# Performance work log

Hardware: AMD Instinct MI355X
Metric: run time of the kernel (lower is better)

The kernel has to match this reference:

```python
import jax, jax.numpy as jnp
import numpy as np

B, E, O, H = 4096, 1024, 16, 1024  # batch, embed_dim, num_ops, hidden_dim


def setup_inputs() -> dict:
    key = jax.random.key(0)
    k1, k2, k3, k4, k5, k6 = jax.random.split(key, 6)
    s1 = 1.0 / np.sqrt(E)
    s2 = 1.0 / np.sqrt(H)
    return {
        "x_aug": jax.random.normal(k1, (B, E), dtype=jnp.float32),
        "op_idx": jax.random.randint(k2, (B,), 0, O, dtype=jnp.int32),
        "W1": jax.random.normal(k3, (E, O, H), dtype=jnp.float32) * s1,  # DenseGeneral kernel: embed -> (ops, hidden)
        "b1": jnp.zeros((O, H), dtype=jnp.float32),
        "W2": jax.random.normal(k4, (H, O, H), dtype=jnp.float32) * s2,  # per-op second layer (diagonal of DenseGeneral)
        "b2": jnp.zeros((O, H), dtype=jnp.float32),
    }


def reference(x_aug, op_idx, W1, b1, W2, b2):
    # h1[b,o,h] = relu(sum_e x[b,e] W1[e,o,h] + b1[o,h])
    h1 = jax.nn.relu(jnp.einsum("be,eoh->boh", x_aug, W1) + b1)
    # h2[b,o,g] = relu(sum_h h1[b,o,h] W2[h,o,g] + b2[o,g])  (per-op MLP)
    h2 = jax.nn.relu(jnp.einsum("boh,hog->bog", h1, W2) + b2)
    # select the chosen operator's output per example
    idx = jnp.broadcast_to(op_idx[:, None, None], (x_aug.shape[0], 1, h2.shape[-1]))
    return jnp.take_along_axis(h2, idx, axis=1).squeeze(1)  # [B, H]
```

## Files before the change

### kernel.cpp

```cpp
#include <hip/hip_runtime.h>

#define Bn 4096
#define En 1024
#define On 16
#define Hn 1024
#define MT 80

using floatx4 = __attribute__((ext_vector_type(4))) float;
using float4v = __attribute__((ext_vector_type(4))) float;
using bf16x8  = __attribute__((ext_vector_type(8))) __bf16;
using short8v = __attribute__((ext_vector_type(8))) short;

__device__ inline unsigned short f2bf(float f) {
    unsigned u = __builtin_bit_cast(unsigned, f);
    u += 0x7fffu + ((u >> 16) & 1u);
    return (unsigned short)(u >> 16);
}

#define GLOAD16(gp, lp) __builtin_amdgcn_global_load_lds( \
    (const __attribute__((address_space(1))) unsigned int*)(gp), \
    (__attribute__((address_space(3))) unsigned int*)(lp), 16, 0, 0)

__global__ __launch_bounds__(256) void wtrans_kernel(const float* __restrict__ W,
                                                     unsigned short* __restrict__ Wt,
                                                     const int* __restrict__ op_idx,
                                                     int* __restrict__ sidx_pad,
                                                     int* __restrict__ offs) {
    if (blockIdx.z == On) {
        if (blockIdx.x != 0 || blockIdx.y != 0) return;
        __shared__ int cnt[On], cur[On], po[On + 1];
        int tid = threadIdx.x;
        if (tid < On) { cnt[tid] = 0; cur[tid] = 0; }
        __syncthreads();
        for (int i = tid; i < Bn; i += 256) atomicAdd(&cnt[op_idx[i]], 1);
        __syncthreads();
        if (tid == 0) {
            int ps = 0;
            for (int o = 0; o < On; ++o) { po[o] = ps; ps += (cnt[o] + 63) & ~63; }
            po[On] = ps;
        }
        __syncthreads();
        for (int p = tid; p < MT * 64; p += 256) sidx_pad[p] = -1;
        __syncthreads();
        for (int i = tid; i < Bn; i += 256) {
            int o = op_idx[i];
            sidx_pad[po[o] + atomicAdd(&cur[o], 1)] = i;
        }
        if (tid <= On) offs[tid] = po[tid];
        if (tid < On)  offs[20 + tid] = cnt[tid];
        return;
    }
    __shared__ float tile[64][65];
    int o = blockIdx.z, e0 = blockIdx.y * 64, h0 = blockIdx.x * 64;
    int t = threadIdx.x;
    int er = t >> 4, c4 = (t & 15) * 4;
#pragma unroll
    for (int r = 0; r < 4; ++r) {
        const float* p = W + ((size_t)(e0 + er + 16 * r) * On + o) * Hn + h0 + c4;
        *(float4v*)&tile[er + 16 * r][c4] = *(const float4v*)p;
    }
    __syncthreads();
    int row = t & 63, gl = t >> 6;
#pragma unroll
    for (int r = 0; r < 2; ++r) {
        int ggl = gl + 4 * r;
        short8v v;
#pragma unroll
        for (int j = 0; j < 8; ++j) v[j] = (short)f2bf(tile[ggl * 8 + j][row]);
        int gg = (e0 >> 3) + ggl;
        size_t dst = ((((size_t)o * 8 + (h0 >> 7)) * 128 + gg) * 128 + ((h0 & 64) + row)) * 8;
        *(short8v*)(Wt + dst) = v;
    }
}

__global__ __launch_bounds__(256) void xprep_kernel(const float* __restrict__ x,
                                                    const int* __restrict__ sidx_pad,
                                                    const int* __restrict__ offs,
                                                    unsigned short* __restrict__ xs) {
    int p0 = blockIdx.x * 64;
    if (p0 >= offs[On]) return;
    int t = threadIdx.x, row = t & 63, gl = t >> 6;
    int src = sidx_pad[p0 + row];
    const float* xr = (src >= 0) ? (x + (size_t)src * En) : nullptr;
    unsigned short* xbase = xs + (size_t)(p0 >> 6) * 65536 + row * 8;
#pragma unroll 4
    for (int r = 0; r < 32; ++r) {
        int gg = gl + r * 4;
        short8v v = {};
        if (xr) {
            float4v f0 = *(const float4v*)(xr + gg * 8);
            float4v f1 = *(const float4v*)(xr + gg * 8 + 4);
#pragma unroll
            for (int j = 0; j < 4; ++j) { v[j] = (short)f2bf(f0[j]); v[4 + j] = (short)f2bf(f1[j]); }
        }
        *(short8v*)(xbase + (size_t)gg * 512) = v;
    }
}

__global__ __launch_bounds__(256, 4) void gemm1_kernel(
    const unsigned short* __restrict__ xs, const unsigned short* __restrict__ Wt,
    const float* __restrict__ bias1, const int* __restrict__ offs,
    unsigned short* __restrict__ h1T) {
    int o = blockIdx.z;
    int cnt = offs[20 + o];
    int m0 = blockIdx.y * 64;
    if (m0 >= cnt) return;
    int mtile = (offs[o] >> 6) + blockIdx.y;
    int n0 = blockIdx.x * 128;

    __shared__ unsigned short As[2][8][64][8];
    __shared__ unsigned short Bs[2][8][128][8];

    int tid = threadIdx.x, lane = tid & 63, wave = tid >> 6;
    const unsigned short* Abase = xs + (size_t)mtile * 65536 + lane * 8;
    const unsigned short* Bbase = Wt + ((size_t)o * 8 + (n0 >> 7)) * 131072 + lane * 8;

    floatx4 acc[2][4] = {};
    int wm = (wave >> 1) * 32, wn = (wave & 1) * 64;
    int l15 = lane & 15, kg = lane >> 4;

#pragma unroll
    for (int i = 0; i < 2; ++i) { int g = wave * 2 + i; GLOAD16(Abase + g * 512, &As[0][g][0][0]); }
#pragma unroll
    for (int i = 0; i < 4; ++i) { int idx = wave * 4 + i; int g = idx >> 1, hf = idx & 1;
        GLOAD16(Bbase + g * 1024 + hf * 512, &Bs[0][g][hf * 64][0]); }

    for (int it = 0; it < 16; ++it) {
        int cur = it & 1;
        __syncthreads();
        if (it + 1 < 16) {
            int aoff = (it + 1) * 4096, boff = (it + 1) * 8192;
#pragma unroll
            for (int i = 0; i < 2; ++i) { int g = wave * 2 + i;
                GLOAD16(Abase + aoff + g * 512, &As[cur ^ 1][g][0][0]); }
#pragma unroll
            for (int i = 0; i < 4; ++i) { int idx = wave * 4 + i; int g = idx >> 1, hf = idx & 1;
                GLOAD16(Bbase + boff + g * 1024 + hf * 512, &Bs[cur ^ 1][g][hf * 64][0]); }
        }
#pragma unroll
        for (int ks = 0; ks < 2; ++ks) {
            int g = ks * 4 + kg;
            bf16x8 af[2], bfr[4];
#pragma unroll
            for (int mt = 0; mt < 2; ++mt) af[mt] = *(const bf16x8*)&As[cur][g][wm + mt * 16 + l15][0];
#pragma unroll
            for (int nt = 0; nt < 4; ++nt) bfr[nt] = *(const bf16x8*)&Bs[cur][g][wn + nt * 16 + l15][0];
#pragma unroll
            for (int mt = 0; mt < 2; ++mt)
#pragma unroll
                for (int nt = 0; nt < 4; ++nt)
                    acc[mt][nt] = __builtin_amdgcn_mfma_f32_16x16x32_bf16(af[mt], bfr[nt], acc[mt][nt], 0, 0, 0);
        }
    }
    __syncthreads();

    unsigned short* ep = &As[0][0][0][0];
#pragma unroll
    for (int nt = 0; nt < 4; ++nt) {
        int col = wn + nt * 16 + l15;
        float bv = bias1[o * Hn + n0 + col];
#pragma unroll
        for (int mt = 0; mt < 2; ++mt)
#pragma unroll
            for (int r = 0; r < 4; ++r) {
                int rowl = wm + mt * 16 + kg * 4 + r;
                float v = acc[mt][nt][r] + bv;
                ep[((col >> 3) * 64 + rowl) * 8 + (col & 7)] = f2bf(v > 0.f ? v : 0.f);
            }
    }
    __syncthreads();
    unsigned short* dst = h1T + (size_t)mtile * 65536 + (size_t)(n0 >> 3) * 512;
#pragma unroll
    for (int rr = 0; rr < 4; ++rr) {
        int idx = rr * 256 + tid;
        *(short8v*)(dst + idx * 8) = *(const short8v*)(ep + idx * 8);
    }
}

__global__ __launch_bounds__(256, 4) void gemm2_kernel(
    const unsigned short* __restrict__ h1T, const unsigned short* __restrict__ Wt,
    const float* __restrict__ bias2, const int* __restrict__ sidx_pad,
    const int* __restrict__ offs, float* __restrict__ out) {
    int o = blockIdx.z;
    int cnt = offs[20 + o];
    int m0 = blockIdx.y * 64;
    if (m0 >= cnt) return;
    int mtile = (offs[o] >> 6) + blockIdx.y;
    int n0 = blockIdx.x * 128;

    __shared__ unsigned short As[2][8][64][8];
    __shared__ unsigned short Bs[2][8][128][8];

    int tid = threadIdx.x, lane = tid & 63, wave = tid >> 6;
    const unsigned short* Abase = h1T + (size_t)mtile * 65536 + lane * 8;
    const unsigned short* Bbase = Wt + ((size_t)o * 8 + (n0 >> 7)) * 131072 + lane * 8;

    floatx4 acc[2][4] = {};
    int wm = (wave >> 1) * 32, wn = (wave & 1) * 64;
    int l15 = lane & 15, kg = lane >> 4;

#pragma unroll
    for (int i = 0; i < 2; ++i) { int g = wave * 2 + i; GLOAD16(Abase + g * 512, &As[0][g][0][0]); }
#pragma unroll
    for (int i = 0; i < 4; ++i) { int idx = wave * 4 + i; int g = idx >> 1, hf = idx & 1;
        GLOAD16(Bbase + g * 1024 + hf * 512, &Bs[0][g][hf * 64][0]); }

    for (int it = 0; it < 16; ++it) {
        int cur = it & 1;
        __syncthreads();
        if (it + 1 < 16) {
            int aoff = (it + 1) * 4096, boff = (it + 1) * 8192;
#pragma unroll
            for (int i = 0; i < 2; ++i) { int g = wave * 2 + i;
                GLOAD16(Abase + aoff + g * 512, &As[cur ^ 1][g][0][0]); }
#pragma unroll
            for (int i = 0; i < 4; ++i) { int idx = wave * 4 + i; int g = idx >> 1, hf = idx & 1;
                GLOAD16(Bbase + boff + g * 1024 + hf * 512, &Bs[cur ^ 1][g][hf * 64][0]); }
        }
#pragma unroll
        for (int ks = 0; ks < 2; ++ks) {
            int g = ks * 4 + kg;
            bf16x8 af[2], bfr[4];
#pragma unroll
            for (int mt = 0; mt < 2; ++mt) af[mt] = *(const bf16x8*)&As[cur][g][wm + mt * 16 + l15][0];
#pragma unroll
            for (int nt = 0; nt < 4; ++nt) bfr[nt] = *(const bf16x8*)&Bs[cur][g][wn + nt * 16 + l15][0];
#pragma unroll
            for (int mt = 0; mt < 2; ++mt)
#pragma unroll
                for (int nt = 0; nt < 4; ++nt)
                    acc[mt][nt] = __builtin_amdgcn_mfma_f32_16x16x32_bf16(af[mt], bfr[nt], acc[mt][nt], 0, 0, 0);
        }
    }

    int p0 = offs[o] + m0;
    float bv[4];
#pragma unroll
    for (int nt = 0; nt < 4; ++nt) bv[nt] = bias2[o * Hn + n0 + wn + nt * 16 + l15];
#pragma unroll
    for (int mt = 0; mt < 2; ++mt)
#pragma unroll
        for (int r = 0; r < 4; ++r) {
            int rowl = wm + mt * 16 + kg * 4 + r;
            int b = sidx_pad[p0 + rowl];
            if (b >= 0) {
                float* orow = out + (size_t)b * Hn + n0 + wn + l15;
#pragma unroll
                for (int nt = 0; nt < 4; ++nt) {
                    float v = acc[mt][nt][r] + bv[nt];
                    orow[nt * 16] = v > 0.f ? v : 0.f;
                }
            }
        }
}

extern "C" void kernel_launch(void* const* d_in, const int* in_sizes, int n_in,
                              void* d_out, int out_size, void* d_ws, size_t ws_size,
                              hipStream_t stream) {
    const float* x      = (const float*)d_in[0];
    const int*   op_idx = (const int*)d_in[1];
    const float* W1     = (const float*)d_in[2];
    const float* bias1  = (const float*)d_in[3];
    const float* W2     = (const float*)d_in[4];
    const float* bias2  = (const float*)d_in[5];
    float* out = (float*)d_out;

    char* ws = (char*)d_ws;
    int* offs      = (int*)ws;
    int* sidx_pad  = (int*)(ws + 1024);
    unsigned short* xs  = (unsigned short*)(ws + 65536);
    unsigned short* h1T = (unsigned short*)(ws + 65536 + 10485760);
    unsigned short* Wt  = (unsigned short*)(ws + 65536 + 20971520);

    hipLaunchKernelGGL(wtrans_kernel, dim3(16, 16, On + 1), dim3(256), 0, stream,
                       W1, Wt, op_idx, sidx_pad, offs);
    hipLaunchKernelGGL(xprep_kernel, dim3(MT), dim3(256), 0, stream,
                       x, sidx_pad, offs, xs);
    dim3 grid(8, 64, On);
    hipLaunchKernelGGL(gemm1_kernel, grid, dim3(256), 0, stream,
                       xs, Wt, bias1, offs, h1T);
    hipLaunchKernelGGL(wtrans_kernel, dim3(16, 16, On), dim3(256), 0, stream,
                       W2, Wt, op_idx, sidx_pad, offs);
    hipLaunchKernelGGL(gemm2_kernel, grid, dim3(256), 0, stream,
                       h1T, Wt, bias2, sidx_pad, offs, out);
}
```

Measured before the change: 284.6 us.

## Use compact tile-to-op grid and 64x64 GEMM tiles with separate bucketing kernel

Splits the bucketing step out of the weight-transpose kernel into its own kernel, which also writes a per-M-tile operator map. The GEMMs then launch a compact grid of 16x80 blocks that look up their operator, instead of a sparse 8x64x16 grid where most blocks exit early. Output tiles shrink from 64x128 to 64x64, which gives more blocks and less LDS per block but lower MFMA reuse per load. The weight layout is changed to match the 64-wide N tiles.

```diff
diff --git a/kernel.cpp b/kernel.cpp
--- a/kernel.cpp
+++ b/kernel.cpp
@@ -21,35 +21,39 @@
     (const __attribute__((address_space(1))) unsigned int*)(gp), \
     (__attribute__((address_space(3))) unsigned int*)(lp), 16, 0, 0)
 
+__global__ __launch_bounds__(256) void bucket_kernel(const int* __restrict__ op_idx,
+                                                     int* __restrict__ sidx_pad,
+                                                     int* __restrict__ meta) {
+    __shared__ int cnt[On], cur[On], po[On + 1];
+    int tid = threadIdx.x;
+    if (tid < On) { cnt[tid] = 0; cur[tid] = 0; }
+    __syncthreads();
+    for (int i = tid; i < Bn; i += 256) atomicAdd(&cnt[op_idx[i]], 1);
+    __syncthreads();
+    if (tid == 0) {
+        int ps = 0;
+        for (int o = 0; o < On; ++o) { po[o] = ps; ps += (cnt[o] + 63) & ~63; }
+        po[On] = ps;
+    }
+    __syncthreads();
+    for (int p = tid; p < MT * 64; p += 256) sidx_pad[p] = -1;
+    __syncthreads();
+    for (int i = tid; i < Bn; i += 256) {
+        int o = op_idx[i];
+        sidx_pad[po[o] + atomicAdd(&cur[o], 1)] = i;
+    }
+    if (tid <= On) meta[tid] = po[tid];
+    if (tid < On)  meta[20 + tid] = cnt[tid];
+    if (tid < MT) {
+        int o2 = -1;
+        for (int o = 0; o < On; ++o)
+            if (tid * 64 >= po[o] && tid * 64 < po[o + 1]) o2 = o;
+        meta[40 + tid] = o2;
+    }
+}
+
 __global__ __launch_bounds__(256) void wtrans_kernel(const float* __restrict__ W,
-                                                     unsigned short* __restrict__ Wt,
-                                                     const int* __restrict__ op_idx,
-                                                     int* __restrict__ sidx_pad,
-                                                     int* __restrict__ offs) {
-    if (blockIdx.z == On) {
-        if (blockIdx.x != 0 || blockIdx.y != 0) return;
-        __shared__ int cnt[On], cur[On], po[On + 1];
-        int tid = threadIdx.x;
-        if (tid < On) { cnt[tid] = 0; cur[tid] = 0; }
-        __syncthreads();
-        for (int i = tid; i < Bn; i += 256) atomicAdd(&cnt[op_idx[i]], 1);
-        __syncthreads();
-        if (tid == 0) {
-            int ps = 0;
-            for (int o = 0; o < On; ++o) { po[o] = ps; ps += (cnt[o] + 63) & ~63; }
-            po[On] = ps;
-        }
-        __syncthreads();
-        for (int p = tid; p < MT * 64; p += 256) sidx_pad[p] = -1;
-        __syncthreads();
-        for (int i = tid; i < Bn; i += 256) {
-            int o = op_idx[i];
-            sidx_pad[po[o] + atomicAdd(&cur[o], 1)] = i;
-        }
-        if (tid <= On) offs[tid] = po[tid];
-        if (tid < On)  offs[20 + tid] = cnt[tid];
-        return;
-    }
+                                                     unsigned short* __restrict__ Wt) {
     __shared__ float tile[64][65];
     int o = blockIdx.z, e0 = blockIdx.y * 64, h0 = blockIdx.x * 64;
     int t = threadIdx.x;
@@ -67,18 +71,17 @@
         short8v v;
 #pragma unroll
         for (int j = 0; j < 8; ++j) v[j] = (short)f2bf(tile[ggl * 8 + j][row]);
-        int gg = (e0 >> 3) + ggl;
-        size_t dst = ((((size_t)o * 8 + (h0 >> 7)) * 128 + gg) * 128 + ((h0 & 64) + row)) * 8;
+        size_t dst = (((size_t)o * 16 + (h0 >> 6)) * 128 + (e0 >> 3) + ggl) * 512 + row * 8;
         *(short8v*)(Wt + dst) = v;
     }
 }
 
 __global__ __launch_bounds__(256) void xprep_kernel(const float* __restrict__ x,
                                                     const int* __restrict__ sidx_pad,
-                                                    const int* __restrict__ offs,
+                                                    const int* __restrict__ meta,
                                                     unsigned short* __restrict__ xs) {
     int p0 = blockIdx.x * 64;
-    if (p0 >= offs[On]) return;
+    if (p0 >= meta[On]) return;
     int t = threadIdx.x, row = t & 63, gl = t >> 6;
     int src = sidx_pad[p0 + row];
     const float* xr = (src >= 0) ? (x + (size_t)src * En) : nullptr;
@@ -99,79 +102,74 @@
 
 __global__ __launch_bounds__(256, 4) void gemm1_kernel(
     const unsigned short* __restrict__ xs, const unsigned short* __restrict__ Wt,
-    const float* __restrict__ bias1, const int* __restrict__ offs,
+    const float* __restrict__ bias1, const int* __restrict__ meta,
     unsigned short* __restrict__ h1T) {
-    int o = blockIdx.z;
-    int cnt = offs[20 + o];
-    int m0 = blockIdx.y * 64;
-    if (m0 >= cnt) return;
-    int mtile = (offs[o] >> 6) + blockIdx.y;
-    int n0 = blockIdx.x * 128;
+    int t = blockIdx.y;
+    int o = meta[40 + t];
+    if (o < 0) return;
+    int nb = blockIdx.x;
 
     __shared__ unsigned short As[2][8][64][8];
-    __shared__ unsigned short Bs[2][8][128][8];
+    __shared__ unsigned short Bs[2][8][64][8];
 
     int tid = threadIdx.x, lane = tid & 63, wave = tid >> 6;
-    const unsigned short* Abase = xs + (size_t)mtile * 65536 + lane * 8;
-    const unsigned short* Bbase = Wt + ((size_t)o * 8 + (n0 >> 7)) * 131072 + lane * 8;
-
-    floatx4 acc[2][4] = {};
-    int wm = (wave >> 1) * 32, wn = (wave & 1) * 64;
+    const unsigned short* Ab = xs + (size_t)t * 65536 + lane * 8;
+    const unsigned short* Bb = Wt + ((size_t)o * 16 + nb) * 65536 + lane * 8;
+
+    floatx4 acc[2][2] = {};
+    int wm = (wave & 1) * 32, wn = (wave >> 1) * 32;
     int l15 = lane & 15, kg = lane >> 4;
-
-#pragma unroll
-    for (int i = 0; i < 2; ++i) { int g = wave * 2 + i; GLOAD16(Abase + g * 512, &As[0][g][0][0]); }
-#pragma unroll
-    for (int i = 0; i < 4; ++i) { int idx = wave * 4 + i; int g = idx >> 1, hf = idx & 1;
-        GLOAD16(Bbase + g * 1024 + hf * 512, &Bs[0][g][hf * 64][0]); }
+    int g0 = wave * 2, g1 = wave * 2 + 1;
+
+    GLOAD16(Ab + g0 * 512, &As[0][g0][0][0]);
+    GLOAD16(Ab + g1 * 512, &As[0][g1][0][0]);
+    GLOAD16(Bb + g0 * 512, &Bs[0][g0][0][0]);
+    GLOAD16(Bb + g1 * 512, &Bs[0][g1][0][0]);
+    __syncthreads();
 
     for (int it = 0; it < 16; ++it) {
-        int cur = it & 1;
-        __syncthreads();
-        if (it + 1 < 16) {
-            int aoff = (it + 1) * 4096, boff = (it + 1) * 8192;
-#pragma unroll
-            for (int i = 0; i < 2; ++i) { int g = wave * 2 + i;
-                GLOAD16(Abase + aoff + g * 512, &As[cur ^ 1][g][0][0]); }
-#pragma unroll
-            for (int i = 0; i < 4; ++i) { int idx = wave * 4 + i; int g = idx >> 1, hf = idx & 1;
-                GLOAD16(Bbase + boff + g * 1024 + hf * 512, &Bs[cur ^ 1][g][hf * 64][0]); }
+        int p = it & 1;
+        if (it < 15) {
+            int off = (it + 1) * 4096;
+            GLOAD16(Ab + off + g0 * 512, &As[p ^ 1][g0][0][0]);
+            GLOAD16(Ab + off + g1 * 512, &As[p ^ 1][g1][0][0]);
+            GLOAD16(Bb + off + g0 * 512, &Bs[p ^ 1][g0][0][0]);
+            GLOAD16(Bb + off + g1 * 512, &Bs[p ^ 1][g1][0][0]);
         }
 #pragma unroll
         for (int ks = 0; ks < 2; ++ks) {
             int g = ks * 4 + kg;
-            bf16x8 af[2], bfr[4];
-#pragma unroll
-            for (int mt = 0; mt < 2; ++mt) af[mt] = *(const bf16x8*)&As[cur][g][wm + mt * 16 + l15][0];
-#pragma unroll
-            for (int nt = 0; nt < 4; ++nt) bfr[nt] = *(const bf16x8*)&Bs[cur][g][wn + nt * 16 + l15][0];
-#pragma unroll
-            for (int mt = 0; mt < 2; ++mt)
-#pragma unroll
-                for (int nt = 0; nt < 4; ++nt)
-                    acc[mt][nt] = __builtin_amdgcn_mfma_f32_16x16x32_bf16(af[mt], bfr[nt], acc[mt][nt], 0, 0, 0);
-        }
-    }
-    __syncthreads();
+            bf16x8 a0 = *(const bf16x8*)&As[p][g][wm + l15][0];
+            bf16x8 a1 = *(const bf16x8*)&As[p][g][wm + 16 + l15][0];
+            bf16x8 b0 = *(const bf16x8*)&Bs[p][g][wn + l15][0];
+            bf16x8 b1 = *(const bf16x8*)&Bs[p][g][wn + 16 + l15][0];
+            acc[0][0] = __builtin_amdgcn_mfma_f32_16x16x32_bf16(a0, b0, acc[0][0], 0, 0, 0);
+            acc[0][1] = __builtin_amdgcn_mfma_f32_16x16x32_bf16(a0, b1, acc[0][1], 0, 0, 0);
+            acc[1][0] = __builtin_amdgcn_mfma_f32_16x16x32_bf16(a1, b0, acc[1][0], 0, 0, 0);
+            acc[1][1] = __builtin_amdgcn_mfma_f32_16x16x32_bf16(a1, b1, acc[1][1], 0, 0, 0);
+        }
+        __syncthreads();
+    }
 
     unsigned short* ep = &As[0][0][0][0];
-#pragma unroll
-    for (int nt = 0; nt < 4; ++nt) {
+    int n0 = nb * 64;
+#pragma unroll
+    for (int nt = 0; nt < 2; ++nt) {
         int col = wn + nt * 16 + l15;
         float bv = bias1[o * Hn + n0 + col];
 #pragma unroll
         for (int mt = 0; mt < 2; ++mt)
 #pragma unroll
             for (int r = 0; r < 4; ++r) {
-                int rowl = wm + mt * 16 + kg * 4 + r;
+                int row = wm + mt * 16 + kg * 4 + r;
                 float v = acc[mt][nt][r] + bv;
-                ep[((col >> 3) * 64 + rowl) * 8 + (col & 7)] = f2bf(v > 0.f ? v : 0.f);
+                ep[((col >> 3) * 64 + row) * 8 + (col & 7)] = f2bf(v > 0.f ? v : 0.f);
             }
     }
     __syncthreads();
-    unsigned short* dst = h1T + (size_t)mtile * 65536 + (size_t)(n0 >> 3) * 512;
-#pragma unroll
-    for (int rr = 0; rr < 4; ++rr) {
+    unsigned short* dst = h1T + (size_t)t * 65536 + nb * 4096;
+#pragma unroll
+    for (int rr = 0; rr < 2; ++rr) {
         int idx = rr * 256 + tid;
         *(short8v*)(dst + idx * 8) = *(const short8v*)(ep + idx * 8);
     }
@@ -180,76 +178,69 @@
 __global__ __launch_bounds__(256, 4) void gemm2_kernel(
     const unsigned short* __restrict__ h1T, const unsigned short* __restrict__ Wt,
     const float* __restrict__ bias2, const int* __restrict__ sidx_pad,
-    const int* __restrict__ offs, float* __restrict__ out) {
-    int o = blockIdx.z;
-    int cnt = offs[20 + o];
-    int m0 = blockIdx.y * 64;
-    if (m0 >= cnt) return;
-    int mtile = (offs[o] >> 6) + blockIdx.y;
-    int n0 = blockIdx.x * 128;
+    const int* __restrict__ meta, float* __restrict__ out) {
+    int t = blockIdx.y;
+    int o = meta[40 + t];
+    if (o < 0) return;
+    int nb = blockIdx.x;
 
     __shared__ unsigned short As[2][8][64][8];
-    __shared__ unsigned short Bs[2][8][128][8];
+    __shared__ unsigned short Bs[2][8][64][8];
 
     int tid = threadIdx.x, lane = tid & 63, wave = tid >> 6;
-    const unsigned short* Abase = h1T + (size_t)mtile * 65536 + lane * 8;
-    const unsigned short* Bbase = Wt + ((size_t)o * 8 + (n0 >> 7)) * 131072 + lane * 8;
-
-    floatx4 acc[2][4] = {};
-    int wm = (wave >> 1) * 32, wn = (wave & 1) * 64;
+    const unsigned short* Ab = h1T + (size_t)t * 65536 + lane * 8;
+    const unsigned short* Bb = Wt + ((size_t)o * 16 + nb) * 65536 + lane * 8;
+
+    floatx4 acc[2][2] = {};
+    int wm = (wave & 1) * 32, wn = (wave >> 1) * 32;
     int l15 = lane & 15, kg = lane >> 4;
-
-#pragma unroll
-    for (int i = 0; i < 2; ++i) { int g = wave * 2 + i; GLOAD16(Abase + g * 512, &As[0][g][0][0]); }
-#pragma unroll
-    for (int i = 0; i < 4; ++i) { int idx = wave * 4 + i; int g = idx >> 1, hf = idx & 1;
-        GLOAD16(Bbase + g * 1024 + hf * 512, &Bs[0][g][hf * 64][0]); }
+    int g0 = wave * 2, g1 = wave * 2 + 1;
+
+    GLOAD16(Ab + g0 * 512, &As[0][g0][0][0]);
+    GLOAD16(Ab + g1 * 512, &As[0][g1][0][0]);
+    GLOAD16(Bb + g0 * 512, &Bs[0][g0][0][0]);
+    GLOAD16(Bb + g1 * 512, &Bs[0][g1][0][0]);
+    __syncthreads();
 
     for (int it = 0; it < 16; ++it) {
-        int cur = it & 1;
-        __syncthreads();
-        if (it + 1 < 16) {
-            int aoff = (it + 1) * 4096, boff = (it + 1) * 8192;
-#pragma unroll
-            for (int i = 0; i < 2; ++i) { int g = wave * 2 + i;
-                GLOAD16(Abase + aoff + g * 512, &As[cur ^ 1][g][0][0]); }
-#pragma unroll
-            for (int i = 0; i < 4; ++i) { int idx = wave * 4 + i; int g = idx >> 1, hf = idx & 1;
-                GLOAD16(Bbase + boff + g * 1024 + hf * 512, &Bs[cur ^ 1][g][hf * 64][0]); }
+        int p = it & 1;
+        if (it < 15) {
+            int off = (it + 1) * 4096;
+            GLOAD16(Ab + off + g0 * 512, &As[p ^ 1][g0][0][0]);
+            GLOAD16(Ab + off + g1 * 512, &As[p ^ 1][g1][0][0]);
+            GLOAD16(Bb + off + g0 * 512, &Bs[p ^ 1][g0][0][0]);
+            GLOAD16(Bb + off + g1 * 512, &Bs[p ^ 1][g1][0][0]);
         }
 #pragma unroll
         for (int ks = 0; ks < 2; ++ks) {
             int g = ks * 4 + kg;
-            bf16x8 af[2], bfr[4];
-#pragma unroll
-            for (int mt = 0; mt < 2; ++mt) af[mt] = *(const bf16x8*)&As[cur][g][wm + mt * 16 + l15][0];
-#pragma unroll
-            for (int nt = 0; nt < 4; ++nt) bfr[nt] = *(const bf16x8*)&Bs[cur][g][wn + nt * 16 + l15][0];
-#pragma unroll
-            for (int mt = 0; mt < 2; ++mt)
-#pragma unroll
-                for (int nt = 0; nt < 4; ++nt)
-                    acc[mt][nt] = __builtin_amdgcn_mfma_f32_16x16x32_bf16(af[mt], bfr[nt], acc[mt][nt], 0, 0, 0);
-        }
-    }
-
-    int p0 = offs[o] + m0;
-    float bv[4];
-#pragma unroll
-    for (int nt = 0; nt < 4; ++nt) bv[nt] = bias2[o * Hn + n0 + wn + nt * 16 + l15];
+            bf16x8 a0 = *(const bf16x8*)&As[p][g][wm + l15][0];
+            bf16x8 a1 = *(const bf16x8*)&As[p][g][wm + 16 + l15][0];
+            bf16x8 b0 = *(const bf16x8*)&Bs[p][g][wn + l15][0];
+            bf16x8 b1 = *(const bf16x8*)&Bs[p][g][wn + 16 + l15][0];
+            acc[0][0] = __builtin_amdgcn_mfma_f32_16x16x32_bf16(a0, b0, acc[0][0], 0, 0, 0);
+            acc[0][1] = __builtin_amdgcn_mfma_f32_16x16x32_bf16(a0, b1, acc[0][1], 0, 0, 0);
+            acc[1][0] = __builtin_amdgcn_mfma_f32_16x16x32_bf16(a1, b0, acc[1][0], 0, 0, 0);
+            acc[1][1] = __builtin_amdgcn_mfma_f32_16x16x32_bf16(a1, b1, acc[1][1], 0, 0, 0);
+        }
+        __syncthreads();
+    }
+
+    int n0 = nb * 64;
+    float bv0 = bias2[o * Hn + n0 + wn + l15];
+    float bv1 = bias2[o * Hn + n0 + wn + 16 + l15];
 #pragma unroll
     for (int mt = 0; mt < 2; ++mt)
 #pragma unroll
         for (int r = 0; r < 4; ++r) {
-            int rowl = wm + mt * 16 + kg * 4 + r;
-            int b = sidx_pad[p0 + rowl];
+            int row = wm + mt * 16 + kg * 4 + r;
+            int b = sidx_pad[t * 64 + row];
             if (b >= 0) {
                 float* orow = out + (size_t)b * Hn + n0 + wn + l15;
-#pragma unroll
-                for (int nt = 0; nt < 4; ++nt) {
-                    float v = acc[mt][nt][r] + bv[nt];
-                    orow[nt * 16] = v > 0.f ? v : 0.f;
-                }
+                float v0 = acc[mt][0][r] + bv0;
+                float v1 = acc[mt][1][r] + bv1;
+                orow[0]  = v0 > 0.f ? v0 : 0.f;
+                orow[16] = v1 > 0.f ? v1 : 0.f;
             }
         }
 }
@@ -266,21 +257,21 @@
     float* out = (float*)d_out;
 
     char* ws = (char*)d_ws;
-    int* offs      = (int*)ws;
+    int* meta      = (int*)ws;
     int* sidx_pad  = (int*)(ws + 1024);
     unsigned short* xs  = (unsigned short*)(ws + 65536);
     unsigned short* h1T = (unsigned short*)(ws + 65536 + 10485760);
     unsigned short* Wt  = (unsigned short*)(ws + 65536 + 20971520);
 
-    hipLaunchKernelGGL(wtrans_kernel, dim3(16, 16, On + 1), dim3(256), 0, stream,
-                       W1, Wt, op_idx, sidx_pad, offs);
+    hipLaunchKernelGGL(bucket_kernel, dim3(1), dim3(256), 0, stream,
+                       op_idx, sidx_pad, meta);
+    hipLaunchKernelGGL(wtrans_kernel, dim3(16, 16, On), dim3(256), 0, stream, W1, Wt);
     hipLaunchKernelGGL(xprep_kernel, dim3(MT), dim3(256), 0, stream,
-                       x, sidx_pad, offs, xs);
-    dim3 grid(8, 64, On);
+                       x, sidx_pad, meta, xs);
+    dim3 grid(16, MT);
     hipLaunchKernelGGL(gemm1_kernel, grid, dim3(256), 0, stream,
-                       xs, Wt, bias1, offs, h1T);
-    hipLaunchKernelGGL(wtrans_kernel, dim3(16, 16, On), dim3(256), 0, stream,
-                       W2, Wt, op_idx, sidx_pad, offs);
+                       xs, Wt, bias1, meta, h1T);
+    hipLaunchKernelGGL(wtrans_kernel, dim3(16, 16, On), dim3(256), 0, stream, W2, Wt);
     hipLaunchKernelGGL(gemm2_kernel, grid, dim3(256), 0, stream,
-                       h1T, Wt, bias2, sidx_pad, offs, out);
-}
+                       h1T, Wt, bias2, sidx_pad, meta, out);
+}
```

Measured after the change: 288.3 us. Within noise of the previous version (+1.3%).
